# Kernel optimization log

Hardware: AMD Instinct MI355X
Metric: run time of the kernel (lower is better)

## Reference

```python
import jax, jax.numpy as jnp
import numpy as np

T, H = 4096, 7168          # tokens, hidden size
Q_LORA, KV_LORA = 1536, 512
ROPE, NOPE, NH = 64, 128, 16
QK = NOPE + ROPE
MAXPOS, SLOTS = 8192, 16384
EPS = 1e-6


def _build_cos_sin_cache():
    # rotary cache layout used by the module: [max_pos, rope] = cos_half || sin_half
    half = ROPE // 2
    inv_freq = 1.0 / (10000.0 ** (np.arange(0, half, dtype=np.float32) / half))
    t = np.arange(MAXPOS, dtype=np.float32)
    freqs = np.outer(t, inv_freq)  # [MAXPOS, half]
    return jnp.asarray(np.concatenate([np.cos(freqs), np.sin(freqs)], axis=-1))


def setup_inputs() -> dict:
    key = jax.random.key(0)
    ks = jax.random.split(key, 8)
    return {
        "hidden_states": jax.random.normal(ks[0], (T, H), jnp.float32),
        "positions": jax.random.randint(ks[1], (T,), 0, MAXPOS, jnp.int32),
        "w_qkv_a": jax.random.normal(ks[2], (H, Q_LORA + KV_LORA + ROPE), jnp.float32) * 0.02,
        "q_a_ln_w": jnp.ones((Q_LORA,), jnp.float32),
        "w_q_b": jax.random.normal(ks[3], (Q_LORA, NH * QK), jnp.float32) * 0.02,
        "kv_a_ln_w": jnp.ones((KV_LORA,), jnp.float32),
        "w_kc": jax.random.normal(ks[4], (NH, NOPE, KV_LORA), jnp.float32) * 0.02,
        "cos_sin_cache": _build_cos_sin_cache(),
        "k_cache": jnp.zeros((SLOTS, KV_LORA), jnp.float32),
        "rope_cache": jnp.zeros((SLOTS, ROPE), jnp.float32),
        "slot_mapping": jnp.arange(T, dtype=jnp.int32),
    }


def _rms_norm(x, w, eps=EPS):
    return x * jax.lax.rsqrt(jnp.mean(x * x, axis=-1, keepdims=True) + eps) * w


def _interleave_rope(x, cos, sin):
    # npu_interleave_rope: de-interleave even/odd lanes into halves, then
    # apply neox-style rotation with full-dim (repeated) cos/sin.
    x1 = x[..., 0::2]
    x2 = x[..., 1::2]
    rot = jnp.concatenate([x1, x2], axis=-1)
    h = rot.shape[-1] // 2
    rot_half = jnp.concatenate([-rot[..., h:], rot[..., :h]], axis=-1)
    return rot * cos + rot_half * sin


def reference(hidden_states, positions, w_qkv_a, q_a_ln_w, w_q_b, kv_a_ln_w,
              w_kc, cos_sin_cache, k_cache, rope_cache, slot_mapping):
    # get_sin_cos: gather cache, chunk in halves, repeat each to full rope dim
    cs = cos_sin_cache[positions]                 # [T, ROPE]
    cos, sin = jnp.split(cs, 2, axis=-1)          # [T, ROPE/2] each
    cos = jnp.tile(cos, (1, 2))                   # [T, ROPE]
    sin = jnp.tile(sin, (1, 2))

    # fused qkv_a projection -> q low-rank + latent kv cache
    qkv = hidden_states @ w_qkv_a                 # [T, Q_LORA + KV_LORA + ROPE]
    q_low = qkv[:, :Q_LORA]
    latent = qkv[:, Q_LORA:]

    # q path: RMSNorm -> q_b projection -> per-head split
    q = _rms_norm(q_low, q_a_ln_w)
    q = (q @ w_q_b).reshape(-1, NH, QK)           # [T, NH, QK]
    q_nope, q_pe = q[..., :NOPE], q[..., NOPE:]

    # absorb: q_nope @ w_kc per head -> [T, NH, KV_LORA]
    q_nope = jnp.einsum("thn,hnk->thk", q_nope, w_kc)
    # interleaved rope on q_pe
    q_pe = _interleave_rope(q_pe, cos[:, None, :], sin[:, None, :])

    # kv path (npu_kv_rmsnorm_rope_cache): rmsnorm latent, rope the rope part,
    # scatter both into the paged caches at slot_mapping
    k_nope = _rms_norm(latent[:, :KV_LORA], kv_a_ln_w)     # [T, KV_LORA]
    k_rope = _interleave_rope(latent[:, KV_LORA:], cos, sin)  # [T, ROPE]
    k_cache = k_cache.at[slot_mapping].set(k_nope)
    rope_cache = rope_cache.at[slot_mapping].set(k_rope)

    q_out = jnp.concatenate([q_nope, q_pe], axis=-1)       # [T, NH, KV_LORA+ROPE]
    k_out = jnp.concatenate([k_nope, k_rope], axis=-1)     # [T, KV_LORA+ROPE]
    return q_out, k_out, k_cache, rope_cache
```

## Files before the change

### kernel.cpp

```cpp
#include <hip/hip_runtime.h>
#include <hip/hip_bf16.h>

typedef __bf16 bf16_t;
typedef __bf16 bf16x8 __attribute__((ext_vector_type(8)));
typedef float f32x4 __attribute__((ext_vector_type(4)));
typedef unsigned int uint;

#define T_TOK 4096
#define H_DIM 7168
#define QLORA 1536
#define KVLORA 512
#define ROPE_D 64
#define NOPE_D 128
#define NHEAD 16
#define NQKV 2112
#define NQB  3072
#define EPS_F 1e-6f


__global__ void cast_f32_bf16(const float* __restrict__ in, bf16_t* __restrict__ out, long n8)
{
    long stride = (long)gridDim.x * blockDim.x;
    for (long i = (long)blockIdx.x * blockDim.x + threadIdx.x; i < n8; i += stride) {
        const float4 a = ((const float4*)in)[i * 2];
        const float4 b = ((const float4*)in)[i * 2 + 1];
        bf16x8 v;
        v[0] = (bf16_t)a.x; v[1] = (bf16_t)a.y; v[2] = (bf16_t)a.z; v[3] = (bf16_t)a.w;
        v[4] = (bf16_t)b.x; v[5] = (bf16_t)b.y; v[6] = (bf16_t)b.z; v[7] = (bf16_t)b.w;
        ((bf16x8*)out)[i] = v;
    }
}

__global__ __launch_bounds__(256) void transpose_cast(const float* __restrict__ in,
                                                      bf16_t* __restrict__ out, int R, int C)
{
    __shared__ float tile[32][33];
    const int bx = blockIdx.x * 32;
    const int by = blockIdx.y * 32;
    const int tx = threadIdx.x & 31, ty = threadIdx.x >> 5;
    #pragma unroll
    for (int r = ty; r < 32; r += 8)
        tile[r][tx] = in[(long)(by + r) * C + bx + tx];
    __syncthreads();
    #pragma unroll
    for (int r = ty; r < 32; r += 8)
        out[(long)(bx + r) * R + by + tx] = (bf16_t)tile[tx][r];
}

__device__ inline float block_sum_256(float v)
{
    #pragma unroll
    for (int off = 32; off > 0; off >>= 1) v += __shfl_xor(v, off, 64);
    __shared__ float tmp[4];
    if ((threadIdx.x & 63) == 0) tmp[threadIdx.x >> 6] = v;
    __syncthreads();
    return tmp[0] + tmp[1] + tmp[2] + tmp[3];
}

__global__ __launch_bounds__(256) void rms_q_kernel(const float* __restrict__ qkv,
                                                    const float* __restrict__ qkvB,
                                                    const float* __restrict__ w,
                                                    bf16_t* __restrict__ q_a)
{
    const int t = blockIdx.x;
    const float* x = qkv + (long)t * NQKV;
    float loc[6];
    float ss = 0.f;
    if (qkvB) {
        const float* xB = qkvB + (long)t * NQKV;
        #pragma unroll
        for (int i = 0; i < 6; i++) {
            float v = x[threadIdx.x + 256 * i] + xB[threadIdx.x + 256 * i];
            loc[i] = v; ss += v * v;
        }
    } else {
        #pragma unroll
        for (int i = 0; i < 6; i++) {
            float v = x[threadIdx.x + 256 * i];
            loc[i] = v; ss += v * v;
        }
    }
    ss = block_sum_256(ss);
    const float sc = rsqrtf(ss / (float)QLORA + EPS_F);
    #pragma unroll
    for (int i = 0; i < 6; i++) {
        int idx = threadIdx.x + 256 * i;
        q_a[(long)t * QLORA + idx] = (bf16_t)(loc[i] * sc * w[idx]);
    }
}

__global__ __launch_bounds__(256) void k_side_kernel(const float* __restrict__ qkv,
                                                     const float* __restrict__ qkvB,
                                                     const float* __restrict__ w_kv,
                                                     const float* __restrict__ cos_sin,
                                                     const int* __restrict__ positions,
                                                     const int* __restrict__ slot_map,
                                                     float* __restrict__ k_out,
                                                     float* __restrict__ kc_out,
                                                     float* __restrict__ rc_out)
{
    const int t = blockIdx.x;
    const float* lat = qkv + (long)t * NQKV + QLORA;
    const float* latB = qkvB ? qkvB + (long)t * NQKV + QLORA : nullptr;
    float v0 = lat[threadIdx.x];
    float v1 = lat[threadIdx.x + 256];
    if (latB) { v0 += latB[threadIdx.x]; v1 += latB[threadIdx.x + 256]; }
    float ss = v0 * v0 + v1 * v1;
    ss = block_sum_256(ss);
    const float sc = rsqrtf(ss / (float)KVLORA + EPS_F);
    const int slot = slot_map[t];
    const float a0 = v0 * sc * w_kv[threadIdx.x];
    const float a1 = v1 * sc * w_kv[threadIdx.x + 256];
    k_out[(long)t * 576 + threadIdx.x]        = a0;
    k_out[(long)t * 576 + 256 + threadIdx.x]  = a1;
    kc_out[(long)slot * KVLORA + threadIdx.x]       = a0;
    kc_out[(long)slot * KVLORA + 256 + threadIdx.x] = a1;
    if (threadIdx.x < 32) {
        const int j = threadIdx.x;
        const int pos = positions[t];
        const float c = cos_sin[pos * 64 + j];
        const float s = cos_sin[pos * 64 + 32 + j];
        float x1 = lat[KVLORA + 2 * j];
        float x2 = lat[KVLORA + 2 * j + 1];
        if (latB) { x1 += latB[KVLORA + 2 * j]; x2 += latB[KVLORA + 2 * j + 1]; }
        const float o1 = x1 * c - x2 * s;
        const float o2 = x2 * c + x1 * s;
        k_out[(long)t * 576 + 512 + j]      = o1;
        k_out[(long)t * 576 + 512 + 32 + j] = o2;
        rc_out[(long)slot * 64 + j]      = o1;
        rc_out[(long)slot * 64 + 32 + j] = o2;
    }
}

__global__ __launch_bounds__(256) void split_q_kernel(const float* __restrict__ q_b,
                                                      const float* __restrict__ cos_sin,
                                                      const int* __restrict__ positions,
                                                      bf16_t* __restrict__ q_nope,
                                                      float* __restrict__ q_out)
{
    const int t = blockIdx.x;
    const float* row = q_b + (long)t * NQB;
    #pragma unroll
    for (int i = 0; i < 8; i++) {
        int idx = threadIdx.x + 256 * i;
        int h = idx >> 7, n = idx & 127;
        q_nope[((long)h * T_TOK + t) * NOPE_D + n] = (bf16_t)row[h * 192 + n];
    }
    const int pos = positions[t];
    #pragma unroll
    for (int i = 0; i < 2; i++) {
        int p = threadIdx.x + 256 * i;
        int h = p >> 5, j = p & 31;
        const float c = cos_sin[pos * 64 + j];
        const float s = cos_sin[pos * 64 + 32 + j];
        const float x1 = row[h * 192 + 128 + 2 * j];
        const float x2 = row[h * 192 + 128 + 2 * j + 1];
        q_out[(long)t * 9216 + h * 576 + 512 + j]      = x1 * c - x2 * s;
        q_out[(long)t * 9216 + h * 576 + 512 + 32 + j] = x2 * c + x1 * s;
    }
}

#define GBM 128
#define GBN 128
#define GBK 64

__global__ __launch_bounds__(512) void gemm_mfma(
    const bf16_t* __restrict__ A, int lda, long sA,
    const bf16_t* __restrict__ Bt, int ldb, long sB,
    float* __restrict__ C, int ldc, long sC,
    int K, int N)
{
    __shared__ bf16_t As[2][GBM * GBK];
    __shared__ bf16_t Bs[2][GBN * GBK];

    const int nwg = gridDim.x * gridDim.y;
    const int bid = blockIdx.y * gridDim.x + blockIdx.x;
    const int cpx = nwg >> 3;
    const int swz = (bid & 7) * cpx + (bid >> 3);
    const int bx = swz % gridDim.x;
    const int by = swz / gridDim.x;

    const int tid = threadIdx.x;
    const int lane = tid & 63;
    const int w = tid >> 6;
    const int wr = w >> 2, wc = w & 3;
    const int fr = lane & 15;
    const int kg = lane >> 4;

    const long brow = (long)by * GBM;
    const long bcol = (long)bx * GBN;

    const bf16_t* Ab = A + blockIdx.z * sA + brow * lda;
    const bf16_t* Bb = Bt + blockIdx.z * sB;
    float* Cb = C + blockIdx.z * sC + brow * ldc;

    const int srow = w * 16 + (lane >> 3);
    const int scol = (((lane & 7) ^ (lane >> 3)) * 8);

    const uint rd_sw = (uint)((kg * 16) ^ ((fr & 7) << 4));
    const uint a_base = (uint)(uintptr_t)(&As[0][0]) + (uint)((wr * 64 + fr) * 128) + rd_sw;
    const uint b_base = (uint)(uintptr_t)(&Bs[0][0]) + (uint)((wc * 32 + fr) * 128) + rd_sw;

    f32x4 acc[4][2] = {};

    const int nt = K / GBK;

    auto stage = [&](int buf, int k0) {
        #pragma unroll
        for (int it = 0; it < 2; it++) {
            const int r = srow + it * 8;
            __builtin_amdgcn_global_load_lds(
                (const __attribute__((address_space(1))) void*)(Ab + (long)r * lda + k0 + scol),
                (__attribute__((address_space(3))) void*)(&As[buf][(w * 16 + it * 8) * GBK]),
                16, 0, 0);
        }
        #pragma unroll
        for (int it = 0; it < 2; it++) {
            const int r = srow + it * 8;
            long bn = bcol + r; if (bn >= N) bn = N - 1;
            __builtin_amdgcn_global_load_lds(
                (const __attribute__((address_space(1))) void*)(Bb + bn * ldb + k0 + scol),
                (__attribute__((address_space(3))) void*)(&Bs[buf][(w * 16 + it * 8) * GBK]),
                16, 0, 0);
        }
    };

    stage(0, 0);
    asm volatile("s_waitcnt vmcnt(0)" ::: "memory");
    __builtin_amdgcn_s_barrier();

    int cur = 0;
    for (int t = 0; t < nt; ++t) {
        if (t + 1 < nt) stage(cur ^ 1, (t + 1) * GBK);

        const uint aa  = a_base + (uint)(cur * (GBM * GBK * 2));
        const uint bb  = b_base + (uint)(cur * (GBN * GBK * 2));
        const uint aaX = aa ^ 64u;
        const uint bbX = bb ^ 64u;
        bf16x8 a00, a01, a02, a03, a10, a11, a12, a13, b00, b01, b10, b11;
        asm volatile("ds_read_b128 %0, %1 offset:0"    : "=v"(a00) : "v"(aa));
        asm volatile("ds_read_b128 %0, %1 offset:2048" : "=v"(a01) : "v"(aa));
        asm volatile("ds_read_b128 %0, %1 offset:4096" : "=v"(a02) : "v"(aa));
        asm volatile("ds_read_b128 %0, %1 offset:6144" : "=v"(a03) : "v"(aa));
        asm volatile("ds_read_b128 %0, %1 offset:0"    : "=v"(a10) : "v"(aaX));
        asm volatile("ds_read_b128 %0, %1 offset:2048" : "=v"(a11) : "v"(aaX));
        asm volatile("ds_read_b128 %0, %1 offset:4096" : "=v"(a12) : "v"(aaX));
        asm volatile("ds_read_b128 %0, %1 offset:6144" : "=v"(a13) : "v"(aaX));
        asm volatile("ds_read_b128 %0, %1 offset:0"    : "=v"(b00) : "v"(bb));
        asm volatile("ds_read_b128 %0, %1 offset:2048" : "=v"(b01) : "v"(bb));
        asm volatile("ds_read_b128 %0, %1 offset:0"    : "=v"(b10) : "v"(bbX));
        asm volatile("ds_read_b128 %0, %1 offset:2048" : "=v"(b11) : "v"(bbX));
        asm volatile("s_waitcnt lgkmcnt(0)" ::: "memory");
        __builtin_amdgcn_sched_barrier(0);

        acc[0][0] = __builtin_amdgcn_mfma_f32_16x16x32_bf16(a00, b00, acc[0][0], 0, 0, 0);
        acc[0][1] = __builtin_amdgcn_mfma_f32_16x16x32_bf16(a00, b01, acc[0][1], 0, 0, 0);
        acc[1][0] = __builtin_amdgcn_mfma_f32_16x16x32_bf16(a01, b00, acc[1][0], 0, 0, 0);
        acc[1][1] = __builtin_amdgcn_mfma_f32_16x16x32_bf16(a01, b01, acc[1][1], 0, 0, 0);
        acc[2][0] = __builtin_amdgcn_mfma_f32_16x16x32_bf16(a02, b00, acc[2][0], 0, 0, 0);
        acc[2][1] = __builtin_amdgcn_mfma_f32_16x16x32_bf16(a02, b01, acc[2][1], 0, 0, 0);
        acc[3][0] = __builtin_amdgcn_mfma_f32_16x16x32_bf16(a03, b00, acc[3][0], 0, 0, 0);
        acc[3][1] = __builtin_amdgcn_mfma_f32_16x16x32_bf16(a03, b01, acc[3][1], 0, 0, 0);
        acc[0][0] = __builtin_amdgcn_mfma_f32_16x16x32_bf16(a10, b10, acc[0][0], 0, 0, 0);
        acc[0][1] = __builtin_amdgcn_mfma_f32_16x16x32_bf16(a10, b11, acc[0][1], 0, 0, 0);
        acc[1][0] = __builtin_amdgcn_mfma_f32_16x16x32_bf16(a11, b10, acc[1][0], 0, 0, 0);
        acc[1][1] = __builtin_amdgcn_mfma_f32_16x16x32_bf16(a11, b11, acc[1][1], 0, 0, 0);
        acc[2][0] = __builtin_amdgcn_mfma_f32_16x16x32_bf16(a12, b10, acc[2][0], 0, 0, 0);
        acc[2][1] = __builtin_amdgcn_mfma_f32_16x16x32_bf16(a12, b11, acc[2][1], 0, 0, 0);
        acc[3][0] = __builtin_amdgcn_mfma_f32_16x16x32_bf16(a13, b10, acc[3][0], 0, 0, 0);
        acc[3][1] = __builtin_amdgcn_mfma_f32_16x16x32_bf16(a13, b11, acc[3][1], 0, 0, 0);

        asm volatile("s_waitcnt vmcnt(0)" ::: "memory");
        __builtin_amdgcn_s_barrier();
        cur ^= 1;
    }

    #pragma unroll
    for (int i = 0; i < 4; i++) {
        #pragma unroll
        for (int j = 0; j < 2; j++) {
            const int row0 = wr * 64 + i * 16 + kg * 4;
            const long col = bcol + wc * 32 + j * 16 + fr;
            if (col < N) {
                #pragma unroll
                for (int r = 0; r < 4; r++)
                    Cb[(long)(row0 + r) * ldc + col] = acc[i][j][r];
            }
        }
    }
}


extern "C" void kernel_launch(void* const* d_in, const int* in_sizes, int n_in,
                              void* d_out, int out_size, void* d_ws, size_t ws_size,
                              hipStream_t stream)
{
    const float* hs       = (const float*)d_in[0];
    const int*   positions= (const int*)d_in[1];
    const float* w_qkv_a  = (const float*)d_in[2];
    const float* q_a_ln_w = (const float*)d_in[3];
    const float* w_q_b    = (const float*)d_in[4];
    const float* kv_a_ln_w= (const float*)d_in[5];
    const float* w_kc     = (const float*)d_in[6];
    const float* cos_sin  = (const float*)d_in[7];
    const float* k_cache_in  = (const float*)d_in[8];
    const float* rope_cache_in = (const float*)d_in[9];
    const int*   slot_map = (const int*)d_in[10];

    float* out   = (float*)d_out;
    float* q_out = out;
    float* k_out = out + 37748736;
    float* kc_out = out + 40108032;
    float* rc_out = out + 48496640;

    char* ws = (char*)d_ws;
    bf16_t* hs_bf  = (bf16_t*)(ws + 0);
    bf16_t* wqkvaT = (bf16_t*)(ws + 58720256);
    bf16_t* wqbT   = (bf16_t*)(ws + 88997888);
    bf16_t* wkcT   = (bf16_t*)(ws + 98435072);
    float*  qkv0   = (float*)(ws + 100532224);

    const bool splitk = ws_size >= (size_t)169738240;

    float*  qkv1;
    bf16_t* q_a;
    float*  q_b;
    bf16_t* q_nope;
    if (splitk) {
        qkv1   = (float*)(ws + 135135232);
        q_a    = (bf16_t*)(ws + 0);
        q_b    = (float*)(ws + 12582912);
        q_nope = (bf16_t*)(ws + 135135232);
    } else {
        qkv1   = nullptr;
        q_a    = (bf16_t*)(ws + 135135232);
        q_b    = (float*)(ws + 0);
        q_nope = (bf16_t*)(ws + 100532224);
    }

    hipMemcpyAsync(kc_out, k_cache_in, (size_t)16384 * 512 * 4, hipMemcpyDeviceToDevice, stream);
    hipMemcpyAsync(rc_out, rope_cache_in, (size_t)16384 * 64 * 4, hipMemcpyDeviceToDevice, stream);

    cast_f32_bf16<<<2048, 256, 0, stream>>>(hs, hs_bf, (long)T_TOK * H_DIM / 8);
    transpose_cast<<<dim3(NQKV / 32, H_DIM / 32), 256, 0, stream>>>(w_qkv_a, wqkvaT, H_DIM, NQKV);
    transpose_cast<<<dim3(NQB / 32, QLORA / 32), 256, 0, stream>>>(w_q_b, wqbT, QLORA, NQB);
    transpose_cast<<<dim3(512 / 32, 2048 / 32), 256, 0, stream>>>(w_kc, wkcT, 2048, 512);

    if (splitk) {
        gemm_mfma<<<dim3((NQKV + GBN - 1) / GBN, T_TOK / GBM, 2), 512, 0, stream>>>(
            hs_bf, H_DIM, 3584, wqkvaT, H_DIM, 3584,
            qkv0, NQKV, (long)T_TOK * NQKV, 3584, NQKV);
    } else {
        gemm_mfma<<<dim3((NQKV + GBN - 1) / GBN, T_TOK / GBM, 1), 512, 0, stream>>>(
            hs_bf, H_DIM, 0, wqkvaT, H_DIM, 0, qkv0, NQKV, 0, H_DIM, NQKV);
    }

    rms_q_kernel<<<T_TOK, 256, 0, stream>>>(qkv0, qkv1, q_a_ln_w, q_a);
    k_side_kernel<<<T_TOK, 256, 0, stream>>>(qkv0, qkv1, kv_a_ln_w, cos_sin, positions, slot_map,
                                             k_out, kc_out, rc_out);

    gemm_mfma<<<dim3(NQB / GBN, T_TOK / GBM, 1), 512, 0, stream>>>(
        q_a, QLORA, 0, wqbT, QLORA, 0, q_b, NQB, 0, QLORA, NQB);

    split_q_kernel<<<T_TOK, 256, 0, stream>>>(q_b, cos_sin, positions, q_nope, q_out);

    gemm_mfma<<<dim3(KVLORA / GBN, T_TOK / GBM, NHEAD), 512, 0, stream>>>(
        q_nope, NOPE_D, (long)T_TOK * NOPE_D,
        wkcT, 2048, 128,
        q_out, NHEAD * 576, 576, NOPE_D, KVLORA);
}
```

Baseline: 384.0 us.

## Fuse q_b GEMM epilogue with q split and RoPE, merge norm kernels

Replaces the generic q_b GEMM plus split_q kernel with a dedicated GEMM whose epilogue writes q_nope in bf16 head-major layout and applies interleaved RoPE to q_pe directly into the output. This drops the fp32 q_b intermediate buffer round trip through memory and one kernel launch. The q RMSNorm and k-side norm/rope/cache kernels are also merged into a single per-token kernel. The epilogue now performs scattered stores and per-element cos/sin loads, and uses cross-lane shuffles inside divergent-looking branches.

```diff
diff --git a/kernel.cpp b/kernel.cpp
--- a/kernel.cpp
+++ b/kernel.cpp
@@ -52,65 +52,52 @@
     #pragma unroll
     for (int off = 32; off > 0; off >>= 1) v += __shfl_xor(v, off, 64);
     __shared__ float tmp[4];
+    __syncthreads();
     if ((threadIdx.x & 63) == 0) tmp[threadIdx.x >> 6] = v;
     __syncthreads();
     return tmp[0] + tmp[1] + tmp[2] + tmp[3];
 }
 
-__global__ __launch_bounds__(256) void rms_q_kernel(const float* __restrict__ qkv,
-                                                    const float* __restrict__ qkvB,
-                                                    const float* __restrict__ w,
-                                                    bf16_t* __restrict__ q_a)
+__global__ __launch_bounds__(256) void rmsq_kside_kernel(
+    const float* __restrict__ qkv, const float* __restrict__ qkvB,
+    const float* __restrict__ q_w, const float* __restrict__ kv_w,
+    const float* __restrict__ cos_sin, const int* __restrict__ positions,
+    const int* __restrict__ slot_map,
+    bf16_t* __restrict__ q_a, float* __restrict__ k_out,
+    float* __restrict__ kc_out, float* __restrict__ rc_out)
 {
     const int t = blockIdx.x;
     const float* x = qkv + (long)t * NQKV;
+    const float* xB = qkvB ? qkvB + (long)t * NQKV : nullptr;
+
     float loc[6];
     float ss = 0.f;
-    if (qkvB) {
-        const float* xB = qkvB + (long)t * NQKV;
-        #pragma unroll
-        for (int i = 0; i < 6; i++) {
-            float v = x[threadIdx.x + 256 * i] + xB[threadIdx.x + 256 * i];
-            loc[i] = v; ss += v * v;
-        }
-    } else {
-        #pragma unroll
-        for (int i = 0; i < 6; i++) {
-            float v = x[threadIdx.x + 256 * i];
-            loc[i] = v; ss += v * v;
-        }
-    }
-    ss = block_sum_256(ss);
-    const float sc = rsqrtf(ss / (float)QLORA + EPS_F);
     #pragma unroll
     for (int i = 0; i < 6; i++) {
         int idx = threadIdx.x + 256 * i;
-        q_a[(long)t * QLORA + idx] = (bf16_t)(loc[i] * sc * w[idx]);
-    }
-}
-
-__global__ __launch_bounds__(256) void k_side_kernel(const float* __restrict__ qkv,
-                                                     const float* __restrict__ qkvB,
-                                                     const float* __restrict__ w_kv,
-                                                     const float* __restrict__ cos_sin,
-                                                     const int* __restrict__ positions,
-                                                     const int* __restrict__ slot_map,
-                                                     float* __restrict__ k_out,
-                                                     float* __restrict__ kc_out,
-                                                     float* __restrict__ rc_out)
-{
-    const int t = blockIdx.x;
-    const float* lat = qkv + (long)t * NQKV + QLORA;
-    const float* latB = qkvB ? qkvB + (long)t * NQKV + QLORA : nullptr;
+        float v = x[idx];
+        if (xB) v += xB[idx];
+        loc[i] = v; ss += v * v;
+    }
+    ss = block_sum_256(ss);
+    const float scq = rsqrtf(ss / (float)QLORA + EPS_F);
+    #pragma unroll
+    for (int i = 0; i < 6; i++) {
+        int idx = threadIdx.x + 256 * i;
+        q_a[(long)t * QLORA + idx] = (bf16_t)(loc[i] * scq * q_w[idx]);
+    }
+
+    const float* lat = x + QLORA;
+    const float* latB = xB ? xB + QLORA : nullptr;
     float v0 = lat[threadIdx.x];
     float v1 = lat[threadIdx.x + 256];
     if (latB) { v0 += latB[threadIdx.x]; v1 += latB[threadIdx.x + 256]; }
-    float ss = v0 * v0 + v1 * v1;
-    ss = block_sum_256(ss);
-    const float sc = rsqrtf(ss / (float)KVLORA + EPS_F);
+    float ssk = v0 * v0 + v1 * v1;
+    ssk = block_sum_256(ssk);
+    const float sck = rsqrtf(ssk / (float)KVLORA + EPS_F);
     const int slot = slot_map[t];
-    const float a0 = v0 * sc * w_kv[threadIdx.x];
-    const float a1 = v1 * sc * w_kv[threadIdx.x + 256];
+    const float a0 = v0 * sck * kv_w[threadIdx.x];
+    const float a1 = v1 * sck * kv_w[threadIdx.x + 256];
     k_out[(long)t * 576 + threadIdx.x]        = a0;
     k_out[(long)t * 576 + 256 + threadIdx.x]  = a1;
     kc_out[(long)slot * KVLORA + threadIdx.x]       = a0;
@@ -129,34 +116,6 @@
         k_out[(long)t * 576 + 512 + 32 + j] = o2;
         rc_out[(long)slot * 64 + j]      = o1;
         rc_out[(long)slot * 64 + 32 + j] = o2;
-    }
-}
-
-__global__ __launch_bounds__(256) void split_q_kernel(const float* __restrict__ q_b,
-                                                      const float* __restrict__ cos_sin,
-                                                      const int* __restrict__ positions,
-                                                      bf16_t* __restrict__ q_nope,
-                                                      float* __restrict__ q_out)
-{
-    const int t = blockIdx.x;
-    const float* row = q_b + (long)t * NQB;
-    #pragma unroll
-    for (int i = 0; i < 8; i++) {
-        int idx = threadIdx.x + 256 * i;
-        int h = idx >> 7, n = idx & 127;
-        q_nope[((long)h * T_TOK + t) * NOPE_D + n] = (bf16_t)row[h * 192 + n];
-    }
-    const int pos = positions[t];
-    #pragma unroll
-    for (int i = 0; i < 2; i++) {
-        int p = threadIdx.x + 256 * i;
-        int h = p >> 5, j = p & 31;
-        const float c = cos_sin[pos * 64 + j];
-        const float s = cos_sin[pos * 64 + 32 + j];
-        const float x1 = row[h * 192 + 128 + 2 * j];
-        const float x2 = row[h * 192 + 128 + 2 * j + 1];
-        q_out[(long)t * 9216 + h * 576 + 512 + j]      = x1 * c - x2 * s;
-        q_out[(long)t * 9216 + h * 576 + 512 + 32 + j] = x2 * c + x1 * s;
     }
 }
 
@@ -290,6 +249,147 @@
     }
 }
 
+__global__ __launch_bounds__(512) void gemm2_fused(
+    const bf16_t* __restrict__ A,
+    const bf16_t* __restrict__ Bt,
+    const float* __restrict__ cos_sin,
+    const int* __restrict__ positions,
+    bf16_t* __restrict__ q_nope,
+    float* __restrict__ q_out)
+{
+    __shared__ bf16_t As[2][GBM * GBK];
+    __shared__ bf16_t Bs[2][GBN * GBK];
+
+    const int nwg = gridDim.x * gridDim.y;
+    const int bid = blockIdx.y * gridDim.x + blockIdx.x;
+    const int cpx = nwg >> 3;
+    const int swz = (bid & 7) * cpx + (bid >> 3);
+    const int bx = swz % gridDim.x;
+    const int by = swz / gridDim.x;
+
+    const int tid = threadIdx.x;
+    const int lane = tid & 63;
+    const int w = tid >> 6;
+    const int wr = w >> 2, wc = w & 3;
+    const int fr = lane & 15;
+    const int kg = lane >> 4;
+
+    const int brow = by * GBM;
+    const int bcol = bx * GBN;
+
+    const bf16_t* Ab = A + (long)brow * QLORA;
+    const bf16_t* Bb = Bt + (long)bcol * QLORA;
+
+    const int srow = w * 16 + (lane >> 3);
+    const int scol = (((lane & 7) ^ (lane >> 3)) * 8);
+
+    const uint rd_sw = (uint)((kg * 16) ^ ((fr & 7) << 4));
+    const uint a_base = (uint)(uintptr_t)(&As[0][0]) + (uint)((wr * 64 + fr) * 128) + rd_sw;
+    const uint b_base = (uint)(uintptr_t)(&Bs[0][0]) + (uint)((wc * 32 + fr) * 128) + rd_sw;
+
+    f32x4 acc[4][2] = {};
+
+    const int nt = QLORA / GBK;
+
+    auto stage = [&](int buf, int k0) {
+        #pragma unroll
+        for (int it = 0; it < 2; it++) {
+            const int r = srow + it * 8;
+            __builtin_amdgcn_global_load_lds(
+                (const __attribute__((address_space(1))) void*)(Ab + (long)r * QLORA + k0 + scol),
+                (__attribute__((address_space(3))) void*)(&As[buf][(w * 16 + it * 8) * GBK]),
+                16, 0, 0);
+            __builtin_amdgcn_global_load_lds(
+                (const __attribute__((address_space(1))) void*)(Bb + (long)r * QLORA + k0 + scol),
+                (__attribute__((address_space(3))) void*)(&Bs[buf][(w * 16 + it * 8) * GBK]),
+                16, 0, 0);
+        }
+    };
+
+    stage(0, 0);
+    asm volatile("s_waitcnt vmcnt(0)" ::: "memory");
+    __builtin_amdgcn_s_barrier();
+
+    int cur = 0;
+    for (int t = 0; t < nt; ++t) {
+        if (t + 1 < nt) stage(cur ^ 1, (t + 1) * GBK);
+
+        const uint aa  = a_base + (uint)(cur * (GBM * GBK * 2));
+        const uint bb  = b_base + (uint)(cur * (GBN * GBK * 2));
+        const uint aaX = aa ^ 64u;
+        const uint bbX = bb ^ 64u;
+        bf16x8 a00, a01, a02, a03, a10, a11, a12, a13, b00, b01, b10, b11;
+        asm volatile("ds_read_b128 %0, %1 offset:0"    : "=v"(a00) : "v"(aa));
+        asm volatile("ds_read_b128 %0, %1 offset:2048" : "=v"(a01) : "v"(aa));
+        asm volatile("ds_read_b128 %0, %1 offset:4096" : "=v"(a02) : "v"(aa));
+        asm volatile("ds_read_b128 %0, %1 offset:6144" : "=v"(a03) : "v"(aa));
+        asm volatile("ds_read_b128 %0, %1 offset:0"    : "=v"(a10) : "v"(aaX));
+        asm volatile("ds_read_b128 %0, %1 offset:2048" : "=v"(a11) : "v"(aaX));
+        asm volatile("ds_read_b128 %0, %1 offset:4096" : "=v"(a12) : "v"(aaX));
+        asm volatile("ds_read_b128 %0, %1 offset:6144" : "=v"(a13) : "v"(aaX));
+        asm volatile("ds_read_b128 %0, %1 offset:0"    : "=v"(b00) : "v"(bb));
+        asm volatile("ds_read_b128 %0, %1 offset:2048" : "=v"(b01) : "v"(bb));
+        asm volatile("ds_read_b128 %0, %1 offset:0"    : "=v"(b10) : "v"(bbX));
+        asm volatile("ds_read_b128 %0, %1 offset:2048" : "=v"(b11) : "v"(bbX));
+        asm volatile("s_waitcnt lgkmcnt(0)" ::: "memory");
+        __builtin_amdgcn_sched_barrier(0);
+
+        acc[0][0] = __builtin_amdgcn_mfma_f32_16x16x32_bf16(a00, b00, acc[0][0], 0, 0, 0);
+        acc[0][1] = __builtin_amdgcn_mfma_f32_16x16x32_bf16(a00, b01, acc[0][1], 0, 0, 0);
+        acc[1][0] = __builtin_amdgcn_mfma_f32_16x16x32_bf16(a01, b00, acc[1][0], 0, 0, 0);
+        acc[1][1] = __builtin_amdgcn_mfma_f32_16x16x32_bf16(a01, b01, acc[1][1], 0, 0, 0);
+        acc[2][0] = __builtin_amdgcn_mfma_f32_16x16x32_bf16(a02, b00, acc[2][0], 0, 0, 0);
+        acc[2][1] = __builtin_amdgcn_mfma_f32_16x16x32_bf16(a02, b01, acc[2][1], 0, 0, 0);
+        acc[3][0] = __builtin_amdgcn_mfma_f32_16x16x32_bf16(a03, b00, acc[3][0], 0, 0, 0);
+        acc[3][1] = __builtin_amdgcn_mfma_f32_16x16x32_bf16(a03, b01, acc[3][1], 0, 0, 0);
+        acc[0][0] = __builtin_amdgcn_mfma_f32_16x16x32_bf16(a10, b10, acc[0][0], 0, 0, 0);
+        acc[0][1] = __builtin_amdgcn_mfma_f32_16x16x32_bf16(a10, b11, acc[0][1], 0, 0, 0);
+        acc[1][0] = __builtin_amdgcn_mfma_f32_16x16x32_bf16(a11, b10, acc[1][0], 0, 0, 0);
+        acc[1][1] = __builtin_amdgcn_mfma_f32_16x16x32_bf16(a11, b11, acc[1][1], 0, 0, 0);
+        acc[2][0] = __builtin_amdgcn_mfma_f32_16x16x32_bf16(a12, b10, acc[2][0], 0, 0, 0);
+        acc[2][1] = __builtin_amdgcn_mfma_f32_16x16x32_bf16(a12, b11, acc[2][1], 0, 0, 0);
+        acc[3][0] = __builtin_amdgcn_mfma_f32_16x16x32_bf16(a13, b10, acc[3][0], 0, 0, 0);
+        acc[3][1] = __builtin_amdgcn_mfma_f32_16x16x32_bf16(a13, b11, acc[3][1], 0, 0, 0);
+
+        asm volatile("s_waitcnt vmcnt(0)" ::: "memory");
+        __builtin_amdgcn_s_barrier();
+        cur ^= 1;
+    }
+
+    #pragma unroll
+    for (int i = 0; i < 4; i++) {
+        #pragma unroll
+        for (int j = 0; j < 2; j++) {
+            const int row0 = wr * 64 + i * 16 + kg * 4;
+            const int col  = bcol + wc * 32 + j * 16 + fr;
+            const int h  = col / 192;
+            const int jj = col - h * 192;
+            if (jj < 128) {
+                #pragma unroll
+                for (int r = 0; r < 4; r++) {
+                    const int t = brow + row0 + r;
+                    q_nope[((long)h * T_TOK + t) * NOPE_D + jj] = (bf16_t)acc[i][j][r];
+                }
+            } else {
+                const int idx = jj - 128;
+                const int j2 = idx >> 1;
+                const int odd = idx & 1;
+                #pragma unroll
+                for (int r = 0; r < 4; r++) {
+                    const int t = brow + row0 + r;
+                    const float v = acc[i][j][r];
+                    const float p = __shfl_xor(v, 1, 64);
+                    const int pos = positions[t];
+                    const float c = cos_sin[pos * 64 + j2];
+                    const float s = cos_sin[pos * 64 + 32 + j2];
+                    const float o = odd ? (v * c + p * s) : (v * c - p * s);
+                    q_out[(long)t * 9216 + h * 576 + 512 + (odd ? 32 : 0) + j2] = o;
+                }
+            }
+        }
+    }
+}
+
 
 extern "C" void kernel_launch(void* const* d_in, const int* in_sizes, int n_in,
                               void* d_out, int out_size, void* d_ws, size_t ws_size,
@@ -324,17 +424,14 @@
 
     float*  qkv1;
     bf16_t* q_a;
-    float*  q_b;
     bf16_t* q_nope;
     if (splitk) {
         qkv1   = (float*)(ws + 135135232);
         q_a    = (bf16_t*)(ws + 0);
-        q_b    = (float*)(ws + 12582912);
         q_nope = (bf16_t*)(ws + 135135232);
     } else {
         qkv1   = nullptr;
         q_a    = (bf16_t*)(ws + 135135232);
-        q_b    = (float*)(ws + 0);
         q_nope = (bf16_t*)(ws + 100532224);
     }
 
@@ -355,14 +452,12 @@
             hs_bf, H_DIM, 0, wqkvaT, H_DIM, 0, qkv0, NQKV, 0, H_DIM, NQKV);
     }
 
-    rms_q_kernel<<<T_TOK, 256, 0, stream>>>(qkv0, qkv1, q_a_ln_w, q_a);
-    k_side_kernel<<<T_TOK, 256, 0, stream>>>(qkv0, qkv1, kv_a_ln_w, cos_sin, positions, slot_map,
-                                             k_out, kc_out, rc_out);
-
-    gemm_mfma<<<dim3(NQB / GBN, T_TOK / GBM, 1), 512, 0, stream>>>(
-        q_a, QLORA, 0, wqbT, QLORA, 0, q_b, NQB, 0, QLORA, NQB);
-
-    split_q_kernel<<<T_TOK, 256, 0, stream>>>(q_b, cos_sin, positions, q_nope, q_out);
+    rmsq_kside_kernel<<<T_TOK, 256, 0, stream>>>(qkv0, qkv1, q_a_ln_w, kv_a_ln_w,
+                                                 cos_sin, positions, slot_map,
+                                                 q_a, k_out, kc_out, rc_out);
+
+    gemm2_fused<<<dim3(NQB / GBN, T_TOK / GBM), 512, 0, stream>>>(
+        q_a, wqbT, cos_sin, positions, q_nope, q_out);
 
     gemm_mfma<<<dim3(KVLORA / GBN, T_TOK / GBM, NHEAD), 512, 0, stream>>>(
         q_nope, NOPE_D, (long)T_TOK * NOPE_D,
```

Result: faster. 373.6 us (-2.7%).
